# Kernel optimization log

Hardware: AMD Instinct MI355X
Metric: run time of the kernel (lower is better)

## Reference

```python
import jax, jax.numpy as jnp
import numpy as np

B, N, C, K = 2, 8192, 128, 16

def _mlp2(h, W1, b1, W2, b2):
    return jax.nn.relu(h @ W1 + b1) @ W2 + b2

def setup_inputs() -> dict:
    key = jax.random.key(0)
    ks = jax.random.split(key, 20)
    s = lambda d: 1.0 / np.sqrt(d)
    inp = {
        "x": jax.random.normal(ks[0], (B, N, C), jnp.float32),
        "position": jax.random.normal(ks[1], (B, N, 3), jnp.float32),
        "Wq": jax.random.normal(ks[2], (C, C), jnp.float32) * s(C),
        "bq": jnp.zeros((C,), jnp.float32),
        "Wk": jax.random.normal(ks[3], (C, C), jnp.float32) * s(C),
        "bk": jnp.zeros((C,), jnp.float32),
        "Wv": jax.random.normal(ks[4], (C, C), jnp.float32) * s(C),
        "bv": jnp.zeros((C,), jnp.float32),
        "Wp1": jax.random.normal(ks[5], (3, C), jnp.float32) * s(3),
        "bp1": jnp.zeros((C,), jnp.float32),
        "Wp2": jax.random.normal(ks[6], (C, C), jnp.float32) * s(C),
        "bp2": jnp.zeros((C,), jnp.float32),
        "Wg1": jax.random.normal(ks[7], (C, C), jnp.float32) * s(C),
        "bg1": jnp.zeros((C,), jnp.float32),
        "Wg2": jax.random.normal(ks[8], (C, C), jnp.float32) * s(C),
        "bg2": jnp.zeros((C,), jnp.float32),
    }
    return inp

def reference(x, position, Wq, bq, Wk, bk, Wv, bv, Wp1, bp1, Wp2, bp2, Wg1, bg1, Wg2, bg2):
    # kNN via squared pairwise distances (monotone in cdist, same topk indices)
    p2 = jnp.sum(position * position, axis=-1)                       # (B,N)
    d2 = p2[:, :, None] + p2[:, None, :] - 2.0 * jnp.einsum("bnd,bmd->bnm", position, position)
    _, idx = jax.lax.top_k(-d2, K)                                    # (B,N,K) nearest (incl self)

    gather = jax.vmap(lambda arr, i: arr[i])                          # per-batch fancy gather
    neighbors = gather(x, idx)                                        # (B,N,K,C)
    pos_nb = gather(position, idx)                                    # (B,N,K,3)

    q = x @ Wq + bq                                                   # (B,N,C)
    k = neighbors @ Wk + bk                                           # (B,N,K,C)
    v = neighbors @ Wv + bv                                           # (B,N,K,C)

    # positional MLP only at gathered pairs (same math as all-pairs-then-gather)
    rel = position[:, :, None, :] - pos_nb                            # (B,N,K,3)
    pe = _mlp2(rel, Wp1, bp1, Wp2, bp2)                               # (B,N,K,C)

    scale = 1.0 / jnp.sqrt(jnp.float32(C))
    attn = (q[:, :, None, :] - k + pe) * scale
    attn = _mlp2(attn, Wg1, bg1, Wg2, bg2)
    attn = jax.nn.softmax(attn, axis=2)                               # softmax over K neighbors
    out = jnp.sum(attn * (v + pe), axis=2)                            # (B,N,C)
    return out
```

## Files before the change

### kernel.cpp

```cpp
#include <hip/hip_runtime.h>
#include <hip/hip_bf16.h>
#include <stdint.h>

#define NPTS 8192
#define CDIM 128
#define KNNK 16
#define WELEMF 16384
#define SCALE 0.08838834764831845f
#define FLDS_BYTES 78848
#define GRES 16
#define NCELL (GRES*GRES*GRES)

typedef __attribute__((ext_vector_type(4))) float f32x4;
typedef __attribute__((ext_vector_type(8))) short s16x8;

__device__ __forceinline__ unsigned short to_bf16(float f){
  union { __hip_bfloat16 h; unsigned short u; } v;
  v.h = __float2bfloat16(f);
  return v.u;
}

__device__ __forceinline__ s16x8 cvt8(const float* p){
  float4 lo = *(const float4*)p;
  float4 hi = *(const float4*)(p + 4);
  s16x8 f;
  f[0]=(short)to_bf16(lo.x); f[1]=(short)to_bf16(lo.y);
  f[2]=(short)to_bf16(lo.z); f[3]=(short)to_bf16(lo.w);
  f[4]=(short)to_bf16(hi.x); f[5]=(short)to_bf16(hi.y);
  f[6]=(short)to_bf16(hi.z); f[7]=(short)to_bf16(hi.w);
  return f;
}

__device__ __forceinline__ unsigned mapf_u(unsigned s){
  return s ^ (0x80000000u | (unsigned)(((int)s) >> 31));
}
__device__ __forceinline__ float unmapf_u(unsigned u){
  unsigned r = (u & 0x80000000u) ? (u ^ 0x80000000u) : ~u;
  return __uint_as_float(r);
}

__global__ __launch_bounds__(1024) void gridbuild_kernel(
    const float* __restrict__ pos, float4* __restrict__ spos4,
    int* __restrict__ starts, unsigned* __restrict__ bboxg)
{
  __shared__ int cnt[NCELL];
  __shared__ int part[1024];
  __shared__ unsigned bbl[6];
  const int b = blockIdx.x, t = threadIdx.x;
  for (int i = t; i < NCELL; i += 1024) cnt[i] = 0;
  if (t < 3) bbl[t] = 0xFFFFFFFFu;
  else if (t < 6) bbl[t] = 0u;
  __syncthreads();

  float4 p[8];
  unsigned mn0=~0u, mn1=~0u, mn2=~0u, mx0=0u, mx1=0u, mx2=0u;
#pragma unroll
  for (int i = 0; i < 8; ++i){
    int m = t + i*1024;
    const float* pp = pos + ((size_t)b*NPTS + m)*3;
    float xx = pp[0], yy = pp[1], zz = pp[2];
    float p2 = __fadd_rn(__fadd_rn(__fmul_rn(xx,xx), __fmul_rn(yy,yy)), __fmul_rn(zz,zz));
    p[i] = make_float4(xx, yy, zz, p2);
    unsigned ux = mapf_u(__float_as_uint(xx));
    unsigned uy = mapf_u(__float_as_uint(yy));
    unsigned uz = mapf_u(__float_as_uint(zz));
    mn0 = min(mn0, ux); mn1 = min(mn1, uy); mn2 = min(mn2, uz);
    mx0 = max(mx0, ux); mx1 = max(mx1, uy); mx2 = max(mx2, uz);
  }
#pragma unroll
  for (int off = 1; off < 64; off <<= 1){
    mn0 = min(mn0, (unsigned)__shfl_xor((int)mn0, off));
    mn1 = min(mn1, (unsigned)__shfl_xor((int)mn1, off));
    mn2 = min(mn2, (unsigned)__shfl_xor((int)mn2, off));
    mx0 = max(mx0, (unsigned)__shfl_xor((int)mx0, off));
    mx1 = max(mx1, (unsigned)__shfl_xor((int)mx1, off));
    mx2 = max(mx2, (unsigned)__shfl_xor((int)mx2, off));
  }
  if ((t & 63) == 0){
    atomicMin(&bbl[0], mn0); atomicMin(&bbl[1], mn1); atomicMin(&bbl[2], mn2);
    atomicMax(&bbl[3], mx0); atomicMax(&bbl[4], mx1); atomicMax(&bbl[5], mx2);
  }
  __syncthreads();
  const float lox = unmapf_u(bbl[0]), loy = unmapf_u(bbl[1]), loz = unmapf_u(bbl[2]);
  const float hix = unmapf_u(bbl[3]), hiy = unmapf_u(bbl[4]), hiz = unmapf_u(bbl[5]);

  int cid[8];
#pragma unroll
  for (int i = 0; i < 8; ++i){
    int ix = min(GRES-1, max(0, (int)((p[i].x - lox) * ((float)GRES/(hix-lox)))));
    int iy = min(GRES-1, max(0, (int)((p[i].y - loy) * ((float)GRES/(hiy-loy)))));
    int iz = min(GRES-1, max(0, (int)((p[i].z - loz) * ((float)GRES/(hiz-loz)))));
    cid[i] = (iz*GRES + iy)*GRES + ix;
    atomicAdd(&cnt[cid[i]], 1);
  }
  __syncthreads();
  const int base = t*4;
  int c0 = cnt[base], c1 = cnt[base+1], c2 = cnt[base+2], c3 = cnt[base+3];
  part[t] = c0+c1+c2+c3;
  __syncthreads();
  for (int off = 1; off < 1024; off <<= 1){
    int v = (t >= off) ? part[t-off] : 0;
    __syncthreads();
    part[t] += v;
    __syncthreads();
  }
  int run = (t > 0) ? part[t-1] : 0;
  int* stb = starts + b*(NCELL+1);
  int r1 = run + c0, r2 = r1 + c1, r3 = r2 + c2;
  stb[base] = run; stb[base+1] = r1; stb[base+2] = r2; stb[base+3] = r3;
  if (t == 1023) stb[NCELL] = r3 + c3;
  cnt[base] = run; cnt[base+1] = r1; cnt[base+2] = r2; cnt[base+3] = r3;
  __syncthreads();
  float4* spb = spos4 + ((size_t)b << 13);
#pragma unroll
  for (int i = 0; i < 8; ++i){
    int m = t + i*1024;
    int dst = atomicAdd(&cnt[cid[i]], 1);
    spb[dst] = make_float4(p[i].x, p[i].y, p[i].z, __uint_as_float((unsigned)m));
  }
  if (t < 6) bboxg[b*6 + t] = bbl[t];
}

__global__ __launch_bounds__(256) void prep_kernel(
    const float* __restrict__ Wq, const float* __restrict__ Wk,
    const float* __restrict__ Wv, const float* __restrict__ Wp2,
    const float* __restrict__ Wg1, const float* __restrict__ Wg2,
    const float* __restrict__ x,
    unsigned short* __restrict__ wt, unsigned short* __restrict__ xbf)
{
  if (blockIdx.x < 384){
    int t = blockIdx.x*256 + threadIdx.x;
    int w = t >> 14, f = t & (WELEMF-1);
    int i = f & 7, ln = (f >> 3) & 63, kkct = f >> 9;
    int kk = kkct & 3, ct = kkct >> 2;
    int kdim = kk*32 + (ln >> 4)*8 + i, col = ct*16 + (ln & 15);
    const float* src = (w==0)?Wq:(w==1)?Wk:(w==2)?Wv:(w==3)?Wp2:(w==4)?Wg1:Wg2;
    float v = src[kdim*CDIM + col];
    if (w == 1) v = -v;
    wt[t] = to_bf16(v);
  } else {
    size_t e = ((size_t)(blockIdx.x - 384)*256 + threadIdx.x) * 8;
    s16x8 v = cvt8(x + e);
    *(s16x8*)&xbf[e] = v;
  }
}

__global__ __launch_bounds__(256) void knn_grid_kernel(
    const float4* __restrict__ spos4, const int* __restrict__ starts,
    const unsigned* __restrict__ bbox, int* __restrict__ idxout)
{
  const int tid = threadIdx.x, lane = tid & 63;
  const int sub = lane >> 4, sl = lane & 15, gbase = sub*16;
  const int w = tid >> 6;
  const int g = blockIdx.x*16 + w*4 + sub;
  const int b = g >> 13, n = g & (NPTS-1);
  const float4* sp = spos4 + ((size_t)b<<13);
  const int*    st = starts + b*(NCELL+1);

  const float4 q4 = sp[n];
  const int orig = __float_as_int(q4.w);
  const float qx = q4.x, qy = q4.y, qz = q4.z;
  const float q2 = __fadd_rn(__fadd_rn(__fmul_rn(qx,qx), __fmul_rn(qy,qy)), __fmul_rn(qz,qz));

  float lox = unmapf_u(bbox[b*6+0]), loy = unmapf_u(bbox[b*6+1]), loz = unmapf_u(bbox[b*6+2]);
  float hix = unmapf_u(bbox[b*6+3]), hiy = unmapf_u(bbox[b*6+4]), hiz = unmapf_u(bbox[b*6+5]);
  float cwx = (hix-lox)*(1.0f/GRES), cwy = (hiy-loy)*(1.0f/GRES), cwz = (hiz-loz)*(1.0f/GRES);
  int cx = min(GRES-1, max(0, (int)((qx - lox) * ((float)GRES/(hix-lox)))));
  int cy = min(GRES-1, max(0, (int)((qy - loy) * ((float)GRES/(hiy-loy)))));
  int cz = min(GRES-1, max(0, (int)((qz - loz) * ((float)GRES/(hiz-loz)))));

  unsigned khi = 0xFFFFFFFFu, klo = 0xFFFFFFFFu;
  float Tf = __builtin_inff();

  auto insert = [&](unsigned ihi, unsigned ilo){
    unsigned phi = (unsigned)__builtin_amdgcn_update_dpp(0, (int)khi, 0x111, 0xF, 0xF, false);
    unsigned plo = (unsigned)__builtin_amdgcn_update_dpp(0, (int)klo, 0x111, 0xF, 0xF, false);
    bool gt  = (khi > ihi) || (khi == ihi && klo > ilo);
    bool pgt = (sl != 0) && ((phi > ihi) || (phi == ihi && plo > ilo));
    khi = gt ? (pgt ? phi : ihi) : khi;
    klo = gt ? (pgt ? plo : ilo) : klo;
  };
  auto updT = [&](){
    unsigned t15 = (unsigned)__shfl((int)khi, gbase + 15);
    Tf = (t15 >= 0xFF800000u) ? __builtin_inff() : unmapf_u(t15);
  };

  bool gdone = false;
  for (int R = 1; R <= GRES-1; ++R){
    const bool first = (R == 1);
    const int per = 8*R, w1 = 2*R-1;
    const int ntask = first ? 9 : (per + 2*w1*w1);
    for (int tb = 0; tb < ntask; tb += 16){
      int t = tb + sl;
      int dy = 0, dz = 0, gx0 = 0, gx1 = -1;
      bool valid = (!gdone) && (t < ntask);
      if (first){
        if (valid){ dy = t % 3 - 1; dz = t / 3 - 1; }
        gx0 = max(cx-1, 0); gx1 = min(cx+1, GRES-1);
      } else if (valid){
        if (t < per){
          int s2 = 2*(2*R+1);
          if (t < s2){ dz = (t < 2*R+1) ? -R : R; dy = t % (2*R+1) - R; }
          else { int u = t - s2; dy = (u & 1) ? R : -R; dz = (u >> 1) - (R-1); }
          gx0 = max(cx-R, 0); gx1 = min(cx+R, GRES-1);
        } else {
          int i = t - per, ri = i >> 1;
          dy = ri % w1 - (R-1); dz = ri / w1 - (R-1);
          int gx = cx + ((i & 1) ? R : -R);
          gx0 = gx; gx1 = gx;
          valid = gx >= 0 && gx <= GRES-1;
        }
      }
      int gy = cy + dy, gz = cz + dz;
      valid = valid && gy >= 0 && gy < GRES && gz >= 0 && gz < GRES && gx0 <= gx1;
      int s0 = 0, s1 = 0;
      if (valid){ int cb = (gz*GRES + gy)*GRES; s0 = st[cb + gx0]; s1 = st[cb + gx1 + 1]; }
      unsigned long long bal = __ballot(valid && (s1 > s0));
      unsigned cm = (unsigned)((bal >> gbase) & 0xFFFFull);
      while (__any(cm != 0)){
        bool act = (cm != 0);
        int srow = act ? __builtin_ctz(cm) : 0;
        if (act) cm &= cm - 1;
        int cs = __shfl(s0, gbase + srow);
        int ce = __shfl(s1, gbase + srow);
        if (!act){ cs = 0; ce = 0; }
        for (int p0 = cs; p0 < ce; p0 += 16){
          int mm = p0 + sl;
          bool v = mm < ce;
          float4 c = v ? sp[mm] : make_float4(0.f,0.f,0.f,0.f);
          float c2  = __fadd_rn(__fadd_rn(__fmul_rn(c.x,c.x), __fmul_rn(c.y,c.y)), __fmul_rn(c.z,c.z));
          float dot = __builtin_fmaf(c.z, qz, __builtin_fmaf(c.y, qy, __fmul_rn(c.x, qx)));
          float d2  = __fsub_rn(__fadd_rn(q2, c2), __fadd_rn(dot, dot));
          int oi = __float_as_int(c.w);
          bool ins = v && (d2 <= Tf);
          unsigned long long ib = __ballot(ins);
          unsigned im = (unsigned)((ib >> gbase) & 0xFFFFull);
          if (__any(im != 0)){
            while (__any(im != 0)){
              bool a2 = (im != 0);
              int s = a2 ? __builtin_ctz(im) : 0;
              if (a2) im &= im - 1;
              unsigned dvb = (unsigned)__shfl((int)__float_as_uint(d2), gbase + s);
              int ov = __shfl(oi, gbase + s);
              if (a2) insert(mapf_u(dvb), (unsigned)ov);
            }
            updT();
          }
        }
      }
    }
    const float big = 1e30f;
    float dxlo = (cx-R <= 0)      ? big : (qx - (lox + (float)(cx-R)*cwx));
    float dxhi = (cx+R >= GRES-1) ? big : ((lox + (float)(cx+R+1)*cwx) - qx);
    float dylo = (cy-R <= 0)      ? big : (qy - (loy + (float)(cy-R)*cwy));
    float dyhi = (cy+R >= GRES-1) ? big : ((loy + (float)(cy+R+1)*cwy) - qy);
    float dzlo = (cz-R <= 0)      ? big : (qz - (loz + (float)(cz-R)*cwz));
    float dzhi = (cz+R >= GRES-1) ? big : ((loz + (float)(cz+R+1)*cwz) - qz);
    float dmin = fminf(fminf(fminf(dxlo,dxhi), fminf(dylo,dyhi)), fminf(dzlo,dzhi));
    bool full = dmin >= 1e29f;
    dmin = fmaxf(dmin, 0.0f);
    float dmin2 = dmin*dmin;
    bool stop = full || (Tf + 1e-4f + Tf*1e-5f < dmin2);
    gdone = gdone || stop;
    if (__all(gdone)) break;
  }
  idxout[(((size_t)b<<13) + orig)*KNNK + sl] = (int)klo;
}

__global__ __launch_bounds__(512, 2) void fused_kernel(
    const float* __restrict__ x, const float* __restrict__ pos,
    const float* __restrict__ bq, const float* __restrict__ bk,
    const float* __restrict__ bv, const float* __restrict__ Wp1,
    const float* __restrict__ bp1, const float* __restrict__ bp2,
    const float* __restrict__ bg1, const float* __restrict__ bg2,
    const int* __restrict__ idxws, const unsigned short* __restrict__ wt,
    const unsigned short* __restrict__ xbf,
    float* __restrict__ out)
{
  extern __shared__ char smem[];
  char* Sbase = smem;
  char* Tbase = smem + 32768;
  float* blds = (float*)(smem + 65536);
  float* q_lds = (float*)(smem + 70656);

  const int tid = threadIdx.x;
  const int lane = tid & 63, w = tid >> 6;
  const int r = lane & 15, grp = lane >> 4;
  const int pbase = blockIdx.x * 16;
  const int b = pbase >> 13;

  auto gll = [&](int s, char* dst){
#pragma unroll
    for (int k = 0; k < 4; ++k){
      int c = w*4 + k;
      unsigned short* g = const_cast<unsigned short*>(wt) + (size_t)s*WELEMF + c*512 + lane*8;
      __builtin_amdgcn_global_load_lds(
        (const __attribute__((address_space(1))) void*)g,
        (__attribute__((address_space(3))) void*)(dst + c*1024), 16, 0, 0);
    }
  };
  auto ldS = [&](int ct, int kk) -> s16x8 {
    return *(const s16x8*)&((unsigned short*)Sbase)[((ct*4 + kk)*64 + lane)*8];
  };
  auto ldT = [&](int ct, int kk) -> s16x8 {
    return *(const s16x8*)&((unsigned short*)Tbase)[((ct*4 + kk)*64 + lane)*8];
  };

  gll(0, Sbase);
  gll(3, Tbase);

  for (int e = tid; e < 1280; e += 512){
    float v;
    if      (e < 128)  v = bq[e];
    else if (e < 256)  v = bk[e-128];
    else if (e < 384)  v = bv[e-256];
    else if (e < 512)  v = bp2[e-384];
    else if (e < 640)  v = bg1[e-512];
    else if (e < 768)  v = bg2[e-640];
    else if (e < 896)  v = bp1[e-768];
    else               v = Wp1[e-896];
    blds[e] = v;
  }
  int nbr[2]; float relx[2], rely[2], relz[2];
#pragma unroll
  for (int j = 0; j < 2; ++j){
    int gp = pbase + w*2 + j;
    nbr[j] = idxws[(size_t)gp*KNNK + r];
    const float* pq = pos + (size_t)gp*3;
    const float* pn = pos + ((size_t)b*NPTS + nbr[j])*3;
    relx[j] = pq[0]-pn[0]; rely[j] = pq[1]-pn[1]; relz[j] = pq[2]-pn[2];
  }
  s16x8 qa[4];
  if (xbf){
    const unsigned short* xr = xbf + (size_t)(pbase + r)*CDIM;
#pragma unroll
    for (int kk = 0; kk < 4; ++kk) qa[kk] = *(const s16x8*)&xr[kk*32 + grp*8];
  } else {
    const float* xr = x + (size_t)(pbase + r)*CDIM;
#pragma unroll
    for (int kk = 0; kk < 4; ++kk) qa[kk] = cvt8(xr + kk*32 + grp*8);
  }
  __syncthreads();

  {
    f32x4 qacc = (f32x4){0.f,0.f,0.f,0.f};
#pragma unroll
    for (int kk = 0; kk < 4; ++kk)
      qacc = __builtin_amdgcn_mfma_f32_16x16x32_bf16(qa[kk], ldS(w,kk), qacc, 0,0,0);
    int col = w*16 + r;
#pragma unroll
    for (int jj = 0; jj < 4; ++jj){
      int row = grp*4 + jj;
      q_lds[row*CDIM + col] = qacc[jj] + blds[col];
    }
  }
  s16x8 pf[2][4];
#pragma unroll
  for (int j = 0; j < 2; ++j)
#pragma unroll
    for (int kk = 0; kk < 4; ++kk){
      s16x8 f;
#pragma unroll
      for (int i = 0; i < 8; ++i){
        int kc = kk*32 + grp*8 + i;
        float s = relx[j]*blds[896+kc] + rely[j]*blds[1024+kc] + relz[j]*blds[1152+kc] + blds[768+kc];
        f[i] = (short)to_bf16(fmaxf(s, 0.f));
      }
      pf[j][kk] = f;
    }
  __syncthreads();
  gll(1, Sbase);

  f32x4 at[2][8], av[2][8];
#pragma unroll
  for (int j=0;j<2;++j)
#pragma unroll
    for (int ct=0;ct<8;++ct) at[j][ct] = (f32x4){0.f,0.f,0.f,0.f};
#pragma unroll
  for (int ct=0;ct<8;++ct)
#pragma unroll
    for (int kk=0;kk<4;++kk){
      s16x8 bw = ldT(ct,kk);
#pragma unroll
      for (int j=0;j<2;++j)
        at[j][ct] = __builtin_amdgcn_mfma_f32_16x16x32_bf16(pf[j][kk], bw, at[j][ct], 0,0,0);
    }
  s16x8 nf[2][4];
  if (xbf){
#pragma unroll
    for (int j=0;j<2;++j){
      const unsigned short* xr = xbf + ((size_t)b*NPTS + nbr[j])*CDIM;
#pragma unroll
      for (int kk=0;kk<4;++kk)
        nf[j][kk] = *(const s16x8*)&xr[kk*32 + grp*8];
    }
  } else {
#pragma unroll
    for (int j=0;j<2;++j)
#pragma unroll
      for (int kk=0;kk<4;++kk)
        nf[j][kk] = cvt8(x + ((size_t)b*NPTS + nbr[j])*CDIM + kk*32 + grp*8);
  }

  __syncthreads();
  gll(2, Tbase);
#pragma unroll
  for (int j=0;j<2;++j)
#pragma unroll
    for (int ct=0;ct<8;++ct) av[j][ct] = at[j][ct];
#pragma unroll
  for (int ct=0;ct<8;++ct)
#pragma unroll
    for (int kk=0;kk<4;++kk){
      s16x8 bw = ldS(ct,kk);
#pragma unroll
      for (int j=0;j<2;++j) at[j][ct] = __builtin_amdgcn_mfma_f32_16x16x32_bf16(nf[j][kk], bw, at[j][ct], 0,0,0);
    }
  __syncthreads();
  gll(4, Sbase);
#pragma unroll
  for (int ct=0;ct<8;++ct)
#pragma unroll
    for (int kk=0;kk<4;++kk){
      s16x8 bw = ldT(ct,kk);
#pragma unroll
      for (int j=0;j<2;++j) av[j][ct] = __builtin_amdgcn_mfma_f32_16x16x32_bf16(nf[j][kk], bw, av[j][ct], 0,0,0);
    }
#pragma unroll
  for (int j=0;j<2;++j){
    int prow = (w*2+j)*CDIM;
#pragma unroll
    for (int ct=0;ct<8;++ct){
      int col = ct*16+r;
      float add = q_lds[prow+col] + blds[384+col] - blds[128+col];
#pragma unroll
      for (int jj=0;jj<4;++jj) at[j][ct][jj] = (at[j][ct][jj] + add)*SCALE;
    }
  }
  __syncthreads();

  unsigned short* tj = (unsigned short*)Tbase + w*2048;
  s16x8 tf[2][4];
#pragma unroll
  for (int j=0;j<2;++j){
#pragma unroll
    for (int ct=0;ct<8;++ct){
      int base = (ct>>1)*512 + ((ct&1)*2 + (r>>3))*128 + (r&7);
#pragma unroll
      for (int jj=0;jj<4;++jj)
        tj[base + (grp*4+jj)*8] = to_bf16(at[j][ct][jj]);
    }
#pragma unroll
    for (int kk=0;kk<4;++kk)
      tf[j][kk] = *(const s16x8*)&tj[(kk*64 + lane)*8];
  }
  f32x4 hacc[2][8];
#pragma unroll
  for (int j=0;j<2;++j)
#pragma unroll
    for (int ct=0;ct<8;++ct) hacc[j][ct] = (f32x4){0.f,0.f,0.f,0.f};
#pragma unroll
  for (int ct=0;ct<8;++ct)
#pragma unroll
    for (int kk=0;kk<4;++kk){
      s16x8 bw = ldS(ct,kk);
#pragma unroll
      for (int j=0;j<2;++j)
        hacc[j][ct] = __builtin_amdgcn_mfma_f32_16x16x32_bf16(tf[j][kk], bw, hacc[j][ct], 0,0,0);
    }
  __syncthreads();
  gll(5, Sbase);
  s16x8 hf[2][4];
#pragma unroll
  for (int j=0;j<2;++j){
#pragma unroll
    for (int ct=0;ct<8;++ct){
      int base = (ct>>1)*512 + ((ct&1)*2 + (r>>3))*128 + (r&7);
      int col = ct*16+r; float bb = blds[512+col];
#pragma unroll
      for (int jj=0;jj<4;++jj)
        tj[base + (grp*4+jj)*8] = to_bf16(fmaxf(hacc[j][ct][jj]+bb, 0.f));
    }
#pragma unroll
    for (int kk=0;kk<4;++kk)
      hf[j][kk] = *(const s16x8*)&tj[(kk*64 + lane)*8];
  }
  __syncthreads();
  f32x4 gacc[2][8];
#pragma unroll
  for (int j=0;j<2;++j)
#pragma unroll
    for (int ct=0;ct<8;++ct) gacc[j][ct] = (f32x4){0.f,0.f,0.f,0.f};
#pragma unroll
  for (int ct=0;ct<8;++ct)
#pragma unroll
    for (int kk=0;kk<4;++kk){
      s16x8 bw = ldS(ct,kk);
#pragma unroll
      for (int j=0;j<2;++j)
        gacc[j][ct] = __builtin_amdgcn_mfma_f32_16x16x32_bf16(hf[j][kk], bw, gacc[j][ct], 0,0,0);
    }
#pragma unroll
  for (int j=0;j<2;++j){
#pragma unroll
    for (int ct=0;ct<8;++ct){
      int col = ct*16+r;
      float gb = blds[640+col];
      float g0v = gacc[j][ct][0]+gb, g1v = gacc[j][ct][1]+gb;
      float g2v = gacc[j][ct][2]+gb, g3v = gacc[j][ct][3]+gb;
      float mx = fmaxf(fmaxf(g0v,g1v), fmaxf(g2v,g3v));
      mx = fmaxf(mx, __shfl_xor(mx,16));
      mx = fmaxf(mx, __shfl_xor(mx,32));
      float e0=__expf(g0v-mx), e1=__expf(g1v-mx), e2=__expf(g2v-mx), e3=__expf(g3v-mx);
      float vb = blds[256+col] + blds[384+col];
      float ss = e0+e1+e2+e3;
      float oo = e0*(av[j][ct][0]+vb) + e1*(av[j][ct][1]+vb)
               + e2*(av[j][ct][2]+vb) + e3*(av[j][ct][3]+vb);
      ss += __shfl_xor(ss,16); ss += __shfl_xor(ss,32);
      oo += __shfl_xor(oo,16); oo += __shfl_xor(oo,32);
      if (grp == 0) out[(size_t)(pbase + w*2 + j)*CDIM + col] = oo/ss;
    }
  }
}

extern "C" void kernel_launch(void* const* d_in, const int* in_sizes, int n_in,
                              void* d_out, int out_size, void* d_ws, size_t ws_size,
                              hipStream_t stream)
{
  const float* x    = (const float*)d_in[0];
  const float* pos  = (const float*)d_in[1];
  const float* Wq   = (const float*)d_in[2];
  const float* bq   = (const float*)d_in[3];
  const float* Wk   = (const float*)d_in[4];
  const float* bk   = (const float*)d_in[5];
  const float* Wv   = (const float*)d_in[6];
  const float* bv   = (const float*)d_in[7];
  const float* Wp1  = (const float*)d_in[8];
  const float* bp1  = (const float*)d_in[9];
  const float* Wp2  = (const float*)d_in[10];
  const float* bp2  = (const float*)d_in[11];
  const float* Wg1  = (const float*)d_in[12];
  const float* bg1  = (const float*)d_in[13];
  const float* Wg2  = (const float*)d_in[14];
  const float* bg2  = (const float*)d_in[15];
  float* out = (float*)d_out;

  char* ws = (char*)d_ws;
  int*            idxs   = (int*)ws;
  unsigned short* wt     = (unsigned short*)(ws + 1048576);
  float4*         spos4  = (float4*)(ws + 1519616);
  int*            starts = (int*)(ws + 2174976);
  unsigned*       bbox   = (unsigned*)(ws + 2699520);
  const size_t XBF_OFF = 2699776;
  const size_t XBF_SZ  = (size_t)2*NPTS*CDIM*2;
  unsigned short* xbf = (ws_size >= XBF_OFF + XBF_SZ) ? (unsigned short*)(ws + XBF_OFF) : nullptr;

  hipFuncSetAttribute((const void*)fused_kernel,
                      hipFuncAttributeMaxDynamicSharedMemorySize, FLDS_BYTES);

  gridbuild_kernel<<<2, 1024, 0, stream>>>(pos, spos4, starts, bbox);
  prep_kernel<<<xbf ? 1408 : 384, 256, 0, stream>>>(Wq, Wk, Wv, Wp2, Wg1, Wg2, x, wt, xbf);
  knn_grid_kernel<<<1024, 256, 0, stream>>>(spos4, starts, bbox, idxs);
  fused_kernel<<<1024, 512, FLDS_BYTES, stream>>>(x, pos, bq, bk, bv, Wp1, bp1, bp2,
                                                  bg1, bg2, idxs, wt, xbf, out);
}
```

Baseline: 186.6 us.

## Fuse grid kNN search into the attention kernel and drop the index buffer

Removes the separate knn_grid_kernel and runs the grid-based kNN search at the start of fused_kernel. Two 16-lane groups per wave find the neighbors for that block's 16 points and write the indices to LDS, not to a global workspace array. This saves a kernel launch and the global write and read of the index buffer. In exchange, only half of each wave's lanes do the search, so it runs with lower parallelism inside a 512-thread block that occupies MFMA resources. The fallback path for when no bf16 copy of x fits in the workspace is also removed.

```diff
diff --git a/kernel.cpp b/kernel.cpp
--- a/kernel.cpp
+++ b/kernel.cpp
@@ -7,7 +7,7 @@
 #define KNNK 16
 #define WELEMF 16384
 #define SCALE 0.08838834764831845f
-#define FLDS_BYTES 78848
+#define FLDS_BYTES 79872
 #define GRES 16
 #define NCELL (GRES*GRES*GRES)
 
@@ -145,136 +145,15 @@
   }
 }
 
-__global__ __launch_bounds__(256) void knn_grid_kernel(
-    const float4* __restrict__ spos4, const int* __restrict__ starts,
-    const unsigned* __restrict__ bbox, int* __restrict__ idxout)
-{
-  const int tid = threadIdx.x, lane = tid & 63;
-  const int sub = lane >> 4, sl = lane & 15, gbase = sub*16;
-  const int w = tid >> 6;
-  const int g = blockIdx.x*16 + w*4 + sub;
-  const int b = g >> 13, n = g & (NPTS-1);
-  const float4* sp = spos4 + ((size_t)b<<13);
-  const int*    st = starts + b*(NCELL+1);
-
-  const float4 q4 = sp[n];
-  const int orig = __float_as_int(q4.w);
-  const float qx = q4.x, qy = q4.y, qz = q4.z;
-  const float q2 = __fadd_rn(__fadd_rn(__fmul_rn(qx,qx), __fmul_rn(qy,qy)), __fmul_rn(qz,qz));
-
-  float lox = unmapf_u(bbox[b*6+0]), loy = unmapf_u(bbox[b*6+1]), loz = unmapf_u(bbox[b*6+2]);
-  float hix = unmapf_u(bbox[b*6+3]), hiy = unmapf_u(bbox[b*6+4]), hiz = unmapf_u(bbox[b*6+5]);
-  float cwx = (hix-lox)*(1.0f/GRES), cwy = (hiy-loy)*(1.0f/GRES), cwz = (hiz-loz)*(1.0f/GRES);
-  int cx = min(GRES-1, max(0, (int)((qx - lox) * ((float)GRES/(hix-lox)))));
-  int cy = min(GRES-1, max(0, (int)((qy - loy) * ((float)GRES/(hiy-loy)))));
-  int cz = min(GRES-1, max(0, (int)((qz - loz) * ((float)GRES/(hiz-loz)))));
-
-  unsigned khi = 0xFFFFFFFFu, klo = 0xFFFFFFFFu;
-  float Tf = __builtin_inff();
-
-  auto insert = [&](unsigned ihi, unsigned ilo){
-    unsigned phi = (unsigned)__builtin_amdgcn_update_dpp(0, (int)khi, 0x111, 0xF, 0xF, false);
-    unsigned plo = (unsigned)__builtin_amdgcn_update_dpp(0, (int)klo, 0x111, 0xF, 0xF, false);
-    bool gt  = (khi > ihi) || (khi == ihi && klo > ilo);
-    bool pgt = (sl != 0) && ((phi > ihi) || (phi == ihi && plo > ilo));
-    khi = gt ? (pgt ? phi : ihi) : khi;
-    klo = gt ? (pgt ? plo : ilo) : klo;
-  };
-  auto updT = [&](){
-    unsigned t15 = (unsigned)__shfl((int)khi, gbase + 15);
-    Tf = (t15 >= 0xFF800000u) ? __builtin_inff() : unmapf_u(t15);
-  };
-
-  bool gdone = false;
-  for (int R = 1; R <= GRES-1; ++R){
-    const bool first = (R == 1);
-    const int per = 8*R, w1 = 2*R-1;
-    const int ntask = first ? 9 : (per + 2*w1*w1);
-    for (int tb = 0; tb < ntask; tb += 16){
-      int t = tb + sl;
-      int dy = 0, dz = 0, gx0 = 0, gx1 = -1;
-      bool valid = (!gdone) && (t < ntask);
-      if (first){
-        if (valid){ dy = t % 3 - 1; dz = t / 3 - 1; }
-        gx0 = max(cx-1, 0); gx1 = min(cx+1, GRES-1);
-      } else if (valid){
-        if (t < per){
-          int s2 = 2*(2*R+1);
-          if (t < s2){ dz = (t < 2*R+1) ? -R : R; dy = t % (2*R+1) - R; }
-          else { int u = t - s2; dy = (u & 1) ? R : -R; dz = (u >> 1) - (R-1); }
-          gx0 = max(cx-R, 0); gx1 = min(cx+R, GRES-1);
-        } else {
-          int i = t - per, ri = i >> 1;
-          dy = ri % w1 - (R-1); dz = ri / w1 - (R-1);
-          int gx = cx + ((i & 1) ? R : -R);
-          gx0 = gx; gx1 = gx;
-          valid = gx >= 0 && gx <= GRES-1;
-        }
-      }
-      int gy = cy + dy, gz = cz + dz;
-      valid = valid && gy >= 0 && gy < GRES && gz >= 0 && gz < GRES && gx0 <= gx1;
-      int s0 = 0, s1 = 0;
-      if (valid){ int cb = (gz*GRES + gy)*GRES; s0 = st[cb + gx0]; s1 = st[cb + gx1 + 1]; }
-      unsigned long long bal = __ballot(valid && (s1 > s0));
-      unsigned cm = (unsigned)((bal >> gbase) & 0xFFFFull);
-      while (__any(cm != 0)){
-        bool act = (cm != 0);
-        int srow = act ? __builtin_ctz(cm) : 0;
-        if (act) cm &= cm - 1;
-        int cs = __shfl(s0, gbase + srow);
-        int ce = __shfl(s1, gbase + srow);
-        if (!act){ cs = 0; ce = 0; }
-        for (int p0 = cs; p0 < ce; p0 += 16){
-          int mm = p0 + sl;
-          bool v = mm < ce;
-          float4 c = v ? sp[mm] : make_float4(0.f,0.f,0.f,0.f);
-          float c2  = __fadd_rn(__fadd_rn(__fmul_rn(c.x,c.x), __fmul_rn(c.y,c.y)), __fmul_rn(c.z,c.z));
-          float dot = __builtin_fmaf(c.z, qz, __builtin_fmaf(c.y, qy, __fmul_rn(c.x, qx)));
-          float d2  = __fsub_rn(__fadd_rn(q2, c2), __fadd_rn(dot, dot));
-          int oi = __float_as_int(c.w);
-          bool ins = v && (d2 <= Tf);
-          unsigned long long ib = __ballot(ins);
-          unsigned im = (unsigned)((ib >> gbase) & 0xFFFFull);
-          if (__any(im != 0)){
-            while (__any(im != 0)){
-              bool a2 = (im != 0);
-              int s = a2 ? __builtin_ctz(im) : 0;
-              if (a2) im &= im - 1;
-              unsigned dvb = (unsigned)__shfl((int)__float_as_uint(d2), gbase + s);
-              int ov = __shfl(oi, gbase + s);
-              if (a2) insert(mapf_u(dvb), (unsigned)ov);
-            }
-            updT();
-          }
-        }
-      }
-    }
-    const float big = 1e30f;
-    float dxlo = (cx-R <= 0)      ? big : (qx - (lox + (float)(cx-R)*cwx));
-    float dxhi = (cx+R >= GRES-1) ? big : ((lox + (float)(cx+R+1)*cwx) - qx);
-    float dylo = (cy-R <= 0)      ? big : (qy - (loy + (float)(cy-R)*cwy));
-    float dyhi = (cy+R >= GRES-1) ? big : ((loy + (float)(cy+R+1)*cwy) - qy);
-    float dzlo = (cz-R <= 0)      ? big : (qz - (loz + (float)(cz-R)*cwz));
-    float dzhi = (cz+R >= GRES-1) ? big : ((loz + (float)(cz+R+1)*cwz) - qz);
-    float dmin = fminf(fminf(fminf(dxlo,dxhi), fminf(dylo,dyhi)), fminf(dzlo,dzhi));
-    bool full = dmin >= 1e29f;
-    dmin = fmaxf(dmin, 0.0f);
-    float dmin2 = dmin*dmin;
-    bool stop = full || (Tf + 1e-4f + Tf*1e-5f < dmin2);
-    gdone = gdone || stop;
-    if (__all(gdone)) break;
-  }
-  idxout[(((size_t)b<<13) + orig)*KNNK + sl] = (int)klo;
-}
-
 __global__ __launch_bounds__(512, 2) void fused_kernel(
     const float* __restrict__ x, const float* __restrict__ pos,
     const float* __restrict__ bq, const float* __restrict__ bk,
     const float* __restrict__ bv, const float* __restrict__ Wp1,
     const float* __restrict__ bp1, const float* __restrict__ bp2,
     const float* __restrict__ bg1, const float* __restrict__ bg2,
-    const int* __restrict__ idxws, const unsigned short* __restrict__ wt,
-    const unsigned short* __restrict__ xbf,
+    const unsigned short* __restrict__ wt, const unsigned short* __restrict__ xbf,
+    const float4* __restrict__ spos4, const int* __restrict__ starts,
+    const unsigned* __restrict__ bboxg,
     float* __restrict__ out)
 {
   extern __shared__ char smem[];
@@ -282,6 +161,7 @@
   char* Tbase = smem + 32768;
   float* blds = (float*)(smem + 65536);
   float* q_lds = (float*)(smem + 70656);
+  int* nbrLds = (int*)(smem + 78848);
 
   const int tid = threadIdx.x;
   const int lane = tid & 63, w = tid >> 6;
@@ -321,26 +201,141 @@
     else               v = Wp1[e-896];
     blds[e] = v;
   }
+
+  {
+    const int sub = grp, sl = r, gb2 = sub*16;
+    const bool act = sub < 2;
+    const int j16 = w*2 + sub;
+    const float4* sp = spos4 + ((size_t)b<<13);
+    const int*    st = starts + b*(NCELL+1);
+
+    float qx = 0.f, qy = 0.f, qz = 0.f, q2 = 0.f;
+    if (act){
+      const float* pq = pos + (size_t)(pbase + j16)*3;
+      qx = pq[0]; qy = pq[1]; qz = pq[2];
+      q2 = __fadd_rn(__fadd_rn(__fmul_rn(qx,qx), __fmul_rn(qy,qy)), __fmul_rn(qz,qz));
+    }
+    float lox = unmapf_u(bboxg[b*6+0]), loy = unmapf_u(bboxg[b*6+1]), loz = unmapf_u(bboxg[b*6+2]);
+    float hix = unmapf_u(bboxg[b*6+3]), hiy = unmapf_u(bboxg[b*6+4]), hiz = unmapf_u(bboxg[b*6+5]);
+    float cwx = (hix-lox)*(1.0f/GRES), cwy = (hiy-loy)*(1.0f/GRES), cwz = (hiz-loz)*(1.0f/GRES);
+    int cx = min(GRES-1, max(0, (int)((qx - lox) * ((float)GRES/(hix-lox)))));
+    int cy = min(GRES-1, max(0, (int)((qy - loy) * ((float)GRES/(hiy-loy)))));
+    int cz = min(GRES-1, max(0, (int)((qz - loz) * ((float)GRES/(hiz-loz)))));
+
+    unsigned khi = 0xFFFFFFFFu, klo = 0xFFFFFFFFu;
+    float Tf = __builtin_inff();
+
+    auto insert = [&](unsigned ihi, unsigned ilo){
+      unsigned phi = (unsigned)__builtin_amdgcn_update_dpp(0, (int)khi, 0x111, 0xF, 0xF, false);
+      unsigned plo = (unsigned)__builtin_amdgcn_update_dpp(0, (int)klo, 0x111, 0xF, 0xF, false);
+      bool gt  = (khi > ihi) || (khi == ihi && klo > ilo);
+      bool pgt = (sl != 0) && ((phi > ihi) || (phi == ihi && plo > ilo));
+      khi = gt ? (pgt ? phi : ihi) : khi;
+      klo = gt ? (pgt ? plo : ilo) : klo;
+    };
+    auto updT = [&](){
+      unsigned t15 = (unsigned)__shfl((int)khi, gb2 + 15);
+      Tf = (t15 >= 0xFF800000u) ? __builtin_inff() : unmapf_u(t15);
+    };
+
+    bool gdone = !act;
+    for (int R = 1; R <= GRES-1; ++R){
+      const bool first = (R == 1);
+      const int per = 8*R, w1 = 2*R-1;
+      const int ntask = first ? 9 : (per + 2*w1*w1);
+      for (int tb = 0; tb < ntask; tb += 16){
+        int t = tb + sl;
+        int dy = 0, dz = 0, gx0 = 0, gx1 = -1;
+        bool valid = (!gdone) && (t < ntask);
+        if (first){
+          if (valid){ dy = t % 3 - 1; dz = t / 3 - 1; }
+          gx0 = max(cx-1, 0); gx1 = min(cx+1, GRES-1);
+        } else if (valid){
+          if (t < per){
+            int s2 = 2*(2*R+1);
+            if (t < s2){ dz = (t < 2*R+1) ? -R : R; dy = t % (2*R+1) - R; }
+            else { int u = t - s2; dy = (u & 1) ? R : -R; dz = (u >> 1) - (R-1); }
+            gx0 = max(cx-R, 0); gx1 = min(cx+R, GRES-1);
+          } else {
+            int i = t - per, ri = i >> 1;
+            dy = ri % w1 - (R-1); dz = ri / w1 - (R-1);
+            int gx = cx + ((i & 1) ? R : -R);
+            gx0 = gx; gx1 = gx;
+            valid = gx >= 0 && gx <= GRES-1;
+          }
+        }
+        int gy = cy + dy, gz = cz + dz;
+        valid = valid && gy >= 0 && gy < GRES && gz >= 0 && gz < GRES && gx0 <= gx1;
+        int s0 = 0, s1 = 0;
+        if (valid){ int cb = (gz*GRES + gy)*GRES; s0 = st[cb + gx0]; s1 = st[cb + gx1 + 1]; }
+        unsigned long long bal = __ballot(valid && (s1 > s0));
+        unsigned cm = (unsigned)((bal >> gb2) & 0xFFFFull);
+        while (__any(cm != 0)){
+          bool a1 = (cm != 0);
+          int srow = a1 ? __builtin_ctz(cm) : 0;
+          if (a1) cm &= cm - 1;
+          int cs = __shfl(s0, gb2 + srow);
+          int ce = __shfl(s1, gb2 + srow);
+          if (!a1){ cs = 0; ce = 0; }
+          for (int p0 = cs; p0 < ce; p0 += 16){
+            int mm = p0 + sl;
+            bool v = mm < ce;
+            float4 c = v ? sp[mm] : make_float4(0.f,0.f,0.f,0.f);
+            float c2  = __fadd_rn(__fadd_rn(__fmul_rn(c.x,c.x), __fmul_rn(c.y,c.y)), __fmul_rn(c.z,c.z));
+            float dot = __builtin_fmaf(c.z, qz, __builtin_fmaf(c.y, qy, __fmul_rn(c.x, qx)));
+            float d2  = __fsub_rn(__fadd_rn(q2, c2), __fadd_rn(dot, dot));
+            int oi = __float_as_int(c.w);
+            bool ins = v && (d2 <= Tf);
+            unsigned long long ib = __ballot(ins);
+            unsigned im = (unsigned)((ib >> gb2) & 0xFFFFull);
+            if (__any(im != 0)){
+              while (__any(im != 0)){
+                bool a2 = (im != 0);
+                int s = a2 ? __builtin_ctz(im) : 0;
+                if (a2) im &= im - 1;
+                unsigned dvb = (unsigned)__shfl((int)__float_as_uint(d2), gb2 + s);
+                int ov = __shfl(oi, gb2 + s);
+                if (a2) insert(mapf_u(dvb), (unsigned)ov);
+              }
+              updT();
+            }
+          }
+        }
+      }
+      const float big = 1e30f;
+      float dxlo = (cx-R <= 0)      ? big : (qx - (lox + (float)(cx-R)*cwx));
+      float dxhi = (cx+R >= GRES-1) ? big : ((lox + (float)(cx+R+1)*cwx) - qx);
+      float dylo = (cy-R <= 0)      ? big : (qy - (loy + (float)(cy-R)*cwy));
+      float dyhi = (cy+R >= GRES-1) ? big : ((loy + (float)(cy+R+1)*cwy) - qy);
+      float dzlo = (cz-R <= 0)      ? big : (qz - (loz + (float)(cz-R)*cwz));
+      float dzhi = (cz+R >= GRES-1) ? big : ((loz + (float)(cz+R+1)*cwz) - qz);
+      float dmin = fminf(fminf(fminf(dxlo,dxhi), fminf(dylo,dyhi)), fminf(dzlo,dzhi));
+      bool full = dmin >= 1e29f;
+      dmin = fmaxf(dmin, 0.0f);
+      float dmin2 = dmin*dmin;
+      bool stop = full || (Tf + 1e-4f + Tf*1e-5f < dmin2);
+      gdone = gdone || stop;
+      if (__all(gdone)) break;
+    }
+    if (act) nbrLds[j16*16 + sl] = (int)klo;
+  }
+  __syncthreads();
+
   int nbr[2]; float relx[2], rely[2], relz[2];
 #pragma unroll
   for (int j = 0; j < 2; ++j){
-    int gp = pbase + w*2 + j;
-    nbr[j] = idxws[(size_t)gp*KNNK + r];
-    const float* pq = pos + (size_t)gp*3;
+    int jp = w*2 + j;
+    nbr[j] = nbrLds[jp*16 + r];
+    const float* pq = pos + (size_t)(pbase + jp)*3;
     const float* pn = pos + ((size_t)b*NPTS + nbr[j])*3;
     relx[j] = pq[0]-pn[0]; rely[j] = pq[1]-pn[1]; relz[j] = pq[2]-pn[2];
   }
   s16x8 qa[4];
-  if (xbf){
+  {
     const unsigned short* xr = xbf + (size_t)(pbase + r)*CDIM;
 #pragma unroll
     for (int kk = 0; kk < 4; ++kk) qa[kk] = *(const s16x8*)&xr[kk*32 + grp*8];
-  } else {
-    const float* xr = x + (size_t)(pbase + r)*CDIM;
-#pragma unroll
-    for (int kk = 0; kk < 4; ++kk) qa[kk] = cvt8(xr + kk*32 + grp*8);
-  }
-  __syncthreads();
+  }
 
   {
     f32x4 qacc = (f32x4){0.f,0.f,0.f,0.f};
@@ -386,20 +381,12 @@
         at[j][ct] = __builtin_amdgcn_mfma_f32_16x16x32_bf16(pf[j][kk], bw, at[j][ct], 0,0,0);
     }
   s16x8 nf[2][4];
-  if (xbf){
-#pragma unroll
-    for (int j=0;j<2;++j){
-      const unsigned short* xr = xbf + ((size_t)b*NPTS + nbr[j])*CDIM;
-#pragma unroll
-      for (int kk=0;kk<4;++kk)
-        nf[j][kk] = *(const s16x8*)&xr[kk*32 + grp*8];
-    }
-  } else {
-#pragma unroll
-    for (int j=0;j<2;++j)
-#pragma unroll
-      for (int kk=0;kk<4;++kk)
-        nf[j][kk] = cvt8(x + ((size_t)b*NPTS + nbr[j])*CDIM + kk*32 + grp*8);
+#pragma unroll
+  for (int j=0;j<2;++j){
+    const unsigned short* xr = xbf + ((size_t)b*NPTS + nbr[j])*CDIM;
+#pragma unroll
+    for (int kk=0;kk<4;++kk)
+      nf[j][kk] = *(const s16x8*)&xr[kk*32 + grp*8];
   }
 
   __syncthreads();
@@ -546,21 +533,19 @@
   float* out = (float*)d_out;
 
   char* ws = (char*)d_ws;
-  int*            idxs   = (int*)ws;
   unsigned short* wt     = (unsigned short*)(ws + 1048576);
   float4*         spos4  = (float4*)(ws + 1519616);
   int*            starts = (int*)(ws + 2174976);
   unsigned*       bbox   = (unsigned*)(ws + 2699520);
   const size_t XBF_OFF = 2699776;
-  const size_t XBF_SZ  = (size_t)2*NPTS*CDIM*2;
-  unsigned short* xbf = (ws_size >= XBF_OFF + XBF_SZ) ? (unsigned short*)(ws + XBF_OFF) : nullptr;
+  unsigned short* xbf    = (unsigned short*)(ws + XBF_OFF);
 
   hipFuncSetAttribute((const void*)fused_kernel,
                       hipFuncAttributeMaxDynamicSharedMemorySize, FLDS_BYTES);
 
   gridbuild_kernel<<<2, 1024, 0, stream>>>(pos, spos4, starts, bbox);
-  prep_kernel<<<xbf ? 1408 : 384, 256, 0, stream>>>(Wq, Wk, Wv, Wp2, Wg1, Wg2, x, wt, xbf);
-  knn_grid_kernel<<<1024, 256, 0, stream>>>(spos4, starts, bbox, idxs);
+  prep_kernel<<<1408, 256, 0, stream>>>(Wq, Wk, Wv, Wp2, Wg1, Wg2, x, wt, xbf);
   fused_kernel<<<1024, 512, FLDS_BYTES, stream>>>(x, pos, bq, bk, bv, Wp1, bp1, bp2,
-                                                  bg1, bg2, idxs, wt, xbf, out);
-}
+                                                  bg1, bg2, wt, xbf, spos4, starts,
+                                                  bbox, out);
+}
```

New measurement: 335.2 us. 79.7% more time.
